# Kernel optimization log

Measured on AMD Instinct MI355X. Metric: run time of the kernel, lower is better.

Reference implementation:

```python
import jax, jax.numpy as jnp
import numpy as np
from jax import lax

N_CLS = 3
ALPHA = 2
NMS = True


def _make_level(key, B, A, D, H, W, P, counts):
    k1, k2, k3, k4, k5 = jax.random.split(key, 5)
    C = N_CLS * A
    logit = jax.random.normal(k1, (B, C, D, H, W), dtype=jnp.float32)
    # valid positive coords use d,h,w >= 1 so padded writes to (0,0,0,0) never collide
    a = jax.random.randint(k2, (B, P), 0, A)
    d = jax.random.randint(k3, (B, P), 1, D)
    h = jax.random.randint(k4, (B, P), 1, H)
    w = jax.random.randint(k5, (B, P), 1, W)
    labels = jax.random.randint(jax.random.fold_in(key, 7), (B, P), 0, N_CLS)
    valid = jnp.arange(P)[None, :] < jnp.asarray(counts)[:, None]  # [B,P]
    coord = jnp.stack([a, d, h, w], axis=-1)
    coord = jnp.where(valid[..., None], coord, -1).astype(jnp.int32)
    # ground-truth prob map: -1 = negative, class id (float) at positive voxels
    prob_gt = -jnp.ones((B, A, D, H, W), dtype=jnp.float32)
    cs = jnp.where(valid[..., None], coord, 0)
    b_idx = jnp.arange(B)[:, None]
    vals = jnp.where(valid, labels.astype(jnp.float32), -1.0)
    prob_gt = prob_gt.at[b_idx, cs[..., 0], cs[..., 1], cs[..., 2], cs[..., 3]].set(vals)
    return logit, prob_gt, coord


def setup_inputs() -> dict:
    key = jax.random.key(0)
    kA, kB = jax.random.split(key)
    logit0, prob_gt0, coord0 = _make_level(kA, 4, 3, 64, 64, 64, 128, [128, 64, 32, 0])
    logit1, prob_gt1, coord1 = _make_level(kB, 4, 3, 32, 32, 32, 128, [64, 16, 8, 128])
    weight_cls = jnp.array([1.0, 1.5, 2.0], dtype=jnp.float32)
    return {
        "logit0": logit0, "logit1": logit1,
        "prob_gt0": prob_gt0, "prob_gt1": prob_gt1,
        "coord0": coord0, "coord1": coord1,
        "weight_cls": weight_cls,
    }


def _level_loss(logit, prob_gt, coord_gt, weight_cls):
    B, C, D, H, W = logit.shape
    A = C // N_CLS
    logit = logit.reshape(B, N_CLS, A, D, H, W)
    logp = jax.nn.log_softmax(logit, axis=1)
    nll = -logp                      # [B,N_cls,A,D,H,W]
    prob = jnp.exp(logp)
    nll_neg = nll[:, 0]              # [B,A,D,H,W]
    prob_neg = prob[:, 0]
    negmask = (prob_gt == -1).astype(logit.dtype)
    if NMS:
        mp = lax.reduce_window(nll_neg, -jnp.inf, lax.max,
                               (1, 1, 3, 3, 3), (1, 1, 1, 1, 1),
                               [(0, 0), (0, 0), (1, 1), (1, 1), (1, 1)])
        negmask = negmask * lax.stop_gradient((mp == nll_neg).astype(logit.dtype))
    w_neg = (1.0 - lax.stop_gradient(prob_neg)) ** ALPHA * negmask
    loss_neg = jnp.sum(nll_neg * w_neg)
    count_neg = jnp.sum(w_neg)
    # positives: ragged coord gather, masked instead of per-sample python loop
    valid = coord_gt[:, :, 0] > -1                       # [B,P]
    c = jnp.where(valid[..., None], coord_gt, 0)         # safe coords
    a, d, h, w = c[..., 0], c[..., 1], c[..., 2], c[..., 3]
    b_idx = jnp.arange(B)[:, None]
    cls = prob_gt[b_idx, a, d, h, w].astype(jnp.int32)   # class id at positives
    cls = jnp.where(valid, cls, 0)
    p_t = prob[b_idx, cls, a, d, h, w]
    nll_t = nll[b_idx, cls, a, d, h, w]
    w_pos = ((1.0 - lax.stop_gradient(p_t)) ** ALPHA
             * weight_cls[cls] * valid.astype(logit.dtype))
    loss_pos = jnp.sum(nll_t * w_pos)
    count_pos = jnp.sum(w_pos)
    return loss_pos, loss_neg, count_pos, count_neg


def reference(logit0, logit1, prob_gt0, prob_gt1, coord0, coord1, weight_cls):
    lp0, ln0, cp0, cn0 = _level_loss(logit0, prob_gt0, coord0, weight_cls)
    lp1, ln1, cp1, cn1 = _level_loss(logit1, prob_gt1, coord1, weight_cls)
    return jnp.stack([lp0 + lp1, ln0 + ln1, cp0 + cp1, cn0 + cn1])
```

## Files before the change

### kernel.cpp

```cpp
#include <hip/hip_runtime.h>
#include <math.h>

#define NEG_INF (-INFINITY)

__device__ __forceinline__ float nll3(float l0, float l1, float l2) {
    float m = fmaxf(l0, fmaxf(l1, l2));
    float e0 = __expf(l0 - m);
    float e1 = __expf(l1 - m);
    float e2 = __expf(l2 - m);
    return __logf(e0 + e1 + e2) - (l0 - m);
}

template<int WL, int NR, int TD, int D, int H, int W>
__device__ void neg_strip(int uid, int lane,
                          const float* __restrict__ logit,
                          const float* __restrict__ pg,
                          float2* __restrict__ slot) {
    constexpr int NI = NR + 2;
    constexpr int HG = H / NR;
    constexpr int DT = D / TD;
    const int w = lane & (WL - 1);

    int t = uid;
    const int hg = t % HG; t /= HG;
    const int dt = t % DT; t /= DT;
    const int ba = t;
    const int a = ba % 3, b = ba / 3;
    const int h0 = hg * NR, d0 = dt * TD;

    const long S = (long)D * H * W;
    const float* lb  = logit + ((long)b * 9 + a) * S;
    const long  cs   = 3 * S;
    const float* pgb = pg + (long)ba * S;

    bool hv[NI]; int hoff[NI];
#pragma unroll
    for (int j = 0; j < NI; ++j) {
        int hh = h0 - 1 + j;
        hv[j] = (hh >= 0) && (hh < H);
        hoff[j] = hh * W + w;
    }

    float cur[NI][3] = {}, nxt[NI][3] = {};
    float vm0[NR], vm1[NR], c1r[NR], pgc[NR] = {}, pgn[NR] = {};
#pragma unroll
    for (int r = 0; r < NR; ++r) { vm0[r] = NEG_INF; vm1[r] = NEG_INF; c1r[r] = 0.f; }

    bool dv_cur = (d0 - 1 >= 0);
    if (dv_cur) {
        const float* p0 = lb + (long)(d0 - 1) * (H * W);
#pragma unroll
        for (int j = 0; j < NI; ++j) if (hv[j]) {
            const float* p = p0 + hoff[j];
            cur[j][0] = p[0]; cur[j][1] = p[cs]; cur[j][2] = p[2 * cs];
        }
    }

    float loss = 0.f, cnt = 0.f;

#pragma unroll
    for (int s = 0; s <= TD + 1; ++s) {
        const int d = d0 - 1 + s;
        const int dn = d + 1;
        const bool dv_nxt = (dn < D);
        if (s <= TD) {
            if (dv_nxt) {
                const float* p0 = lb + (long)dn * (H * W);
#pragma unroll
                for (int j = 0; j < NI; ++j) if (hv[j]) {
                    const float* p = p0 + hoff[j];
                    nxt[j][0] = p[0]; nxt[j][1] = p[cs]; nxt[j][2] = p[2 * cs];
                }
            }
            if (s >= 1) {
                const float* pp = pgb + (long)d * (H * W);
#pragma unroll
                for (int r = 0; r < NR; ++r)
                    pgn[r] = pp[(h0 + r) * W + w];
            }
        }

        float nv[NI], rm[NI];
#pragma unroll
        for (int j = 0; j < NI; ++j)
            nv[j] = (dv_cur && hv[j]) ? nll3(cur[j][0], cur[j][1], cur[j][2])
                                      : NEG_INF;
#pragma unroll
        for (int j = 0; j < NI; ++j) {
            float lf = __shfl(nv[j], lane - 1);
            float rt = __shfl(nv[j], lane + 1);
            lf = (w == 0)      ? NEG_INF : lf;
            rt = (w == WL - 1) ? NEG_INF : rt;
            rm[j] = fmaxf(nv[j], fmaxf(lf, rt));
        }
#pragma unroll
        for (int r = 0; r < NR; ++r) {
            float hw2 = fmaxf(rm[r], fmaxf(rm[r + 1], rm[r + 2]));
            float cc  = nv[r + 1];
            if (s >= 2 && pgc[r] == -1.0f) {
                float mp = fmaxf(vm0[r], fmaxf(vm1[r], hw2));
                if (mp == c1r[r]) {
                    float pn = __expf(-c1r[r]);
                    float wn = (1.f - pn) * (1.f - pn);
                    loss += c1r[r] * wn;
                    cnt  += wn;
                }
            }
            vm0[r] = vm1[r]; vm1[r] = hw2; c1r[r] = cc;
        }
#pragma unroll
        for (int r = 0; r < NR; ++r) pgc[r] = pgn[r];
        dv_cur = dv_nxt;
#pragma unroll
        for (int j = 0; j < NI; ++j) {
            cur[j][0] = nxt[j][0]; cur[j][1] = nxt[j][1]; cur[j][2] = nxt[j][2];
        }
    }

#pragma unroll
    for (int off = WL / 2; off > 0; off >>= 1) {
        loss += __shfl_down(loss, off, WL);
        cnt  += __shfl_down(cnt, off, WL);
    }
    if (w == 0) slot[uid] = make_float2(loss, cnt);
}

__device__ void pos_wave8(int sub, int lane,
                          const float* __restrict__ logit,
                          const float* __restrict__ prob_gt,
                          const int* __restrict__ coord,
                          const float* __restrict__ wcls,
                          float2* __restrict__ slot,
                          int D, int H, int W) {
    const int A = 3, P = 128;
    const long S = (long)D * H * W;
    const int i = sub * 64 + lane;
    const int b = i / P;
    const int* c = coord + (long)i * 4;
    const int a = c[0];
    float loss = 0.f, cnt = 0.f;
    if (a > -1) {
        const int d = c[1], h = c[2], w = c[3];
        const long s = ((long)d * H + h) * W + w;
        const int cls = (int)prob_gt[((long)b * A + a) * S + s];
        const float* lp = logit + ((long)b * 3 * A + a) * S + s;
        float l0 = lp[0];
        float l1 = lp[(long)A * S];
        float l2 = lp[2L * A * S];
        float m = fmaxf(l0, fmaxf(l1, l2));
        float e0 = __expf(l0 - m);
        float e1 = __expf(l1 - m);
        float e2 = __expf(l2 - m);
        float lsum = __logf(e0 + e1 + e2);
        float lc = (cls == 0) ? l0 : ((cls == 1) ? l1 : l2);
        float lpc = (lc - m) - lsum;
        float pt = __expf(lpc);
        float wp = (1.f - pt) * (1.f - pt) * wcls[cls];
        loss = (-lpc) * wp;
        cnt = wp;
    }
#pragma unroll
    for (int off = 32; off > 0; off >>= 1) {
        loss += __shfl_down(loss, off);
        cnt  += __shfl_down(cnt, off);
    }
    if (lane == 0) *slot = make_float2(loss, cnt);
}

#define NU0 6144
#define NW0 6144
#define NU1 1536
#define NW1 768
#define NWP 16
#define NSLOT (NU0 + NU1 + NWP)
#define TOTAL_WAVES (NW0 + NW1 + NWP)

__global__ __launch_bounds__(256)
void mega_kernel(const float* __restrict__ logit0,
                 const float* __restrict__ logit1,
                 const float* __restrict__ pg0,
                 const float* __restrict__ pg1,
                 const int* __restrict__ coord0,
                 const int* __restrict__ coord1,
                 const float* __restrict__ wcls,
                 float2* __restrict__ ws) {
    const int gw = blockIdx.x * 4 + (threadIdx.x >> 6);
    const int lane = threadIdx.x & 63;
    float2* wsneg = ws;
    float2* wspos = ws + (NU0 + NU1);
    if (gw < NW0) {
        neg_strip<64, 2, 4, 64, 64, 64>(gw, lane, logit0, pg0, wsneg);
    } else if (gw < NW0 + NW1) {
        const int u = (gw - NW0) * 2 + (lane >> 5);
        neg_strip<32, 2, 4, 32, 32, 32>(u, lane, logit1, pg1, wsneg + NU0);
    } else if (gw < NW0 + NW1 + 8) {
        const int sub = gw - NW0 - NW1;
        pos_wave8(sub, lane, logit0, pg0, coord0, wcls, wspos + sub, 64, 64, 64);
    } else if (gw < NW0 + NW1 + 16) {
        const int sub = gw - NW0 - NW1 - 8;
        pos_wave8(sub, lane, logit1, pg1, coord1, wcls, wspos + 8 + sub, 32, 32, 32);
    }
}

__global__ __launch_bounds__(1024)
void final_reduce(const float2* __restrict__ ws, float* __restrict__ out) {
    const float2* wsneg = ws;
    const float2* wspos = ws + (NU0 + NU1);
    float ln = 0.f, cn = 0.f, lp = 0.f, cp = 0.f;
    for (int i = threadIdx.x; i < NU0 + NU1; i += 1024) {
        float2 v = wsneg[i]; ln += v.x; cn += v.y;
    }
    if (threadIdx.x < NWP) {
        float2 v = wspos[threadIdx.x]; lp = v.x; cp = v.y;
    }
#pragma unroll
    for (int off = 32; off > 0; off >>= 1) {
        ln += __shfl_down(ln, off); cn += __shfl_down(cn, off);
        lp += __shfl_down(lp, off); cp += __shfl_down(cp, off);
    }
    __shared__ float s[16][4];
    const int wv = threadIdx.x >> 6;
    if ((threadIdx.x & 63) == 0) {
        s[wv][0] = ln; s[wv][1] = cn; s[wv][2] = lp; s[wv][3] = cp;
    }
    __syncthreads();
    if (threadIdx.x == 0) {
        float a = 0.f, b = 0.f, c = 0.f, d = 0.f;
#pragma unroll
        for (int i = 0; i < 16; ++i) {
            a += s[i][0]; b += s[i][1]; c += s[i][2]; d += s[i][3];
        }
        out[0] = c;
        out[1] = a;
        out[2] = d;
        out[3] = b;
    }
}

extern "C" void kernel_launch(void* const* d_in, const int* in_sizes, int n_in,
                              void* d_out, int out_size, void* d_ws, size_t ws_size,
                              hipStream_t stream) {
    const float* logit0   = (const float*)d_in[0];
    const float* logit1   = (const float*)d_in[1];
    const float* prob_gt0 = (const float*)d_in[2];
    const float* prob_gt1 = (const float*)d_in[3];
    const int*   coord0   = (const int*)d_in[4];
    const int*   coord1   = (const int*)d_in[5];
    const float* wcls     = (const float*)d_in[6];
    float* out = (float*)d_out;
    float2* ws = (float2*)d_ws;

    mega_kernel<<<TOTAL_WAVES / 4, 256, 0, stream>>>(
        logit0, logit1, prob_gt0, prob_gt1, coord0, coord1, wcls, ws);
    final_reduce<<<1, 1024, 0, stream>>>(ws, out);
}
```

Before: 106.7 us.

## Vectorize negative NMS strips with float4 loads and cross-row shuffles

Each lane now handles four consecutive W positions via float4 loads, and the wave is split into groups that each own one H row. The 3x3 H-neighbourhood max is formed with lane shuffles across groups instead of each lane loading all NR+2 rows. Level 1 now uses NR=4 so a full 64-lane wave is used per unit. The aim is fewer load instructions and less redundant row loading. In exchange it adds more shuffles and leaves some lanes idle, since only NR of the NR+2 groups accumulate.

```diff
diff --git a/kernel.cpp b/kernel.cpp
--- a/kernel.cpp
+++ b/kernel.cpp
@@ -11,15 +11,18 @@
     return __logf(e0 + e1 + e2) - (l0 - m);
 }
 
-template<int WL, int NR, int TD, int D, int H, int W>
-__device__ void neg_strip(int uid, int lane,
-                          const float* __restrict__ logit,
-                          const float* __restrict__ pg,
-                          float2* __restrict__ slot) {
+template<int W, int NR, int TD, int D, int H>
+__device__ void neg_strip_v(int uid, int lane,
+                            const float* __restrict__ logit,
+                            const float* __restrict__ pg,
+                            float2* __restrict__ slot) {
+    constexpr int LR = W / 4;
+    constexpr int NG = 64 / LR;
     constexpr int NI = NR + 2;
     constexpr int HG = H / NR;
     constexpr int DT = D / TD;
-    const int w = lane & (WL - 1);
+    const int q = lane % LR;
+    const int g = lane / LR;
 
     int t = uid;
     const int hg = t % HG; t /= HG;
@@ -33,27 +36,25 @@
     const long  cs   = 3 * S;
     const float* pgb = pg + (long)ba * S;
 
-    bool hv[NI]; int hoff[NI];
-#pragma unroll
-    for (int j = 0; j < NI; ++j) {
-        int hh = h0 - 1 + j;
-        hv[j] = (hh >= 0) && (hh < H);
-        hoff[j] = hh * W + w;
-    }
-
-    float cur[NI][3] = {}, nxt[NI][3] = {};
-    float vm0[NR], vm1[NR], c1r[NR], pgc[NR] = {}, pgn[NR] = {};
-#pragma unroll
-    for (int r = 0; r < NR; ++r) { vm0[r] = NEG_INF; vm1[r] = NEG_INF; c1r[r] = 0.f; }
-
-    bool dv_cur = (d0 - 1 >= 0);
-    if (dv_cur) {
-        const float* p0 = lb + (long)(d0 - 1) * (H * W);
-#pragma unroll
-        for (int j = 0; j < NI; ++j) if (hv[j]) {
-            const float* p = p0 + hoff[j];
-            cur[j][0] = p[0]; cur[j][1] = p[cs]; cur[j][2] = p[2 * cs];
-        }
+    const int jrow = h0 - 1 + g;
+    const bool hv = (jrow >= 0) && (jrow < H) && (g < NI);
+    const int hcl = min(max(jrow, 0), H - 1);
+    const int rowoff = hcl * W + 4 * q;
+    const int prowoff = (h0 + min(g, NR - 1)) * W + 4 * q;
+
+    float4 c0, c1v, c2, n0, n1, n2, pgn;
+    bool dvc = (d0 - 1 >= 0);
+    {
+        const float* p = lb + (long)max(d0 - 1, 0) * (H * W) + rowoff;
+        c0  = *(const float4*)(p);
+        c1v = *(const float4*)(p + cs);
+        c2  = *(const float4*)(p + 2 * cs);
+    }
+
+    float vm0[4], vm1[4], cc1[4], pgc[4];
+#pragma unroll
+    for (int i = 0; i < 4; ++i) {
+        vm0[i] = NEG_INF; vm1[i] = NEG_INF; cc1[i] = 0.f; pgc[i] = 0.f;
     }
 
     float loss = 0.f, cnt = 0.f;
@@ -61,68 +62,68 @@
 #pragma unroll
     for (int s = 0; s <= TD + 1; ++s) {
         const int d = d0 - 1 + s;
-        const int dn = d + 1;
-        const bool dv_nxt = (dn < D);
+        const bool dvn = (s <= TD - 1) || (d + 1 < D);
         if (s <= TD) {
-            if (dv_nxt) {
-                const float* p0 = lb + (long)dn * (H * W);
-#pragma unroll
-                for (int j = 0; j < NI; ++j) if (hv[j]) {
-                    const float* p = p0 + hoff[j];
-                    nxt[j][0] = p[0]; nxt[j][1] = p[cs]; nxt[j][2] = p[2 * cs];
-                }
-            }
-            if (s >= 1) {
-                const float* pp = pgb + (long)d * (H * W);
-#pragma unroll
-                for (int r = 0; r < NR; ++r)
-                    pgn[r] = pp[(h0 + r) * W + w];
-            }
-        }
-
-        float nv[NI], rm[NI];
-#pragma unroll
-        for (int j = 0; j < NI; ++j)
-            nv[j] = (dv_cur && hv[j]) ? nll3(cur[j][0], cur[j][1], cur[j][2])
-                                      : NEG_INF;
-#pragma unroll
-        for (int j = 0; j < NI; ++j) {
-            float lf = __shfl(nv[j], lane - 1);
-            float rt = __shfl(nv[j], lane + 1);
-            lf = (w == 0)      ? NEG_INF : lf;
-            rt = (w == WL - 1) ? NEG_INF : rt;
-            rm[j] = fmaxf(nv[j], fmaxf(lf, rt));
-        }
-#pragma unroll
-        for (int r = 0; r < NR; ++r) {
-            float hw2 = fmaxf(rm[r], fmaxf(rm[r + 1], rm[r + 2]));
-            float cc  = nv[r + 1];
-            if (s >= 2 && pgc[r] == -1.0f) {
-                float mp = fmaxf(vm0[r], fmaxf(vm1[r], hw2));
-                if (mp == c1r[r]) {
-                    float pn = __expf(-c1r[r]);
+            const float* p = lb + (long)min(d + 1, D - 1) * (H * W) + rowoff;
+            n0 = *(const float4*)(p);
+            n1 = *(const float4*)(p + cs);
+            n2 = *(const float4*)(p + 2 * cs);
+            pgn = *(const float4*)(pgb + (long)min(max(d, 0), D - 1) * (H * W)
+                                   + prowoff);
+        }
+
+        float nvv[4];
+        {
+            const bool vv = dvc && hv;
+            nvv[0] = vv ? nll3(c0.x, c1v.x, c2.x) : NEG_INF;
+            nvv[1] = vv ? nll3(c0.y, c1v.y, c2.y) : NEG_INF;
+            nvv[2] = vv ? nll3(c0.z, c1v.z, c2.z) : NEG_INF;
+            nvv[3] = vv ? nll3(c0.w, c1v.w, c2.w) : NEG_INF;
+        }
+
+        float le = __shfl(nvv[3], lane - 1);
+        float re = __shfl(nvv[0], lane + 1);
+        le = (q == 0)      ? NEG_INF : le;
+        re = (q == LR - 1) ? NEG_INF : re;
+        float rm[4];
+        rm[0] = fmaxf(le,     fmaxf(nvv[0], nvv[1]));
+        rm[1] = fmaxf(nvv[0], fmaxf(nvv[1], nvv[2]));
+        rm[2] = fmaxf(nvv[1], fmaxf(nvv[2], nvv[3]));
+        rm[3] = fmaxf(nvv[2], fmaxf(nvv[3], re));
+
+        float rmA[4], rmB[4], ctr[4];
+#pragma unroll
+        for (int i = 0; i < 4; ++i) {
+            rmA[i] = __shfl(rm[i],  lane + LR);
+            rmB[i] = __shfl(rm[i],  lane + 2 * LR);
+            ctr[i] = __shfl(nvv[i], lane + LR);
+        }
+
+#pragma unroll
+        for (int i = 0; i < 4; ++i) {
+            float hw2 = fmaxf(rm[i], fmaxf(rmA[i], rmB[i]));
+            if (s >= 2 && g < NR && pgc[i] == -1.0f) {
+                float mp = fmaxf(vm0[i], fmaxf(vm1[i], hw2));
+                if (mp == cc1[i]) {
+                    float pn = __expf(-cc1[i]);
                     float wn = (1.f - pn) * (1.f - pn);
-                    loss += c1r[r] * wn;
+                    loss += cc1[i] * wn;
                     cnt  += wn;
                 }
             }
-            vm0[r] = vm1[r]; vm1[r] = hw2; c1r[r] = cc;
-        }
-#pragma unroll
-        for (int r = 0; r < NR; ++r) pgc[r] = pgn[r];
-        dv_cur = dv_nxt;
-#pragma unroll
-        for (int j = 0; j < NI; ++j) {
-            cur[j][0] = nxt[j][0]; cur[j][1] = nxt[j][1]; cur[j][2] = nxt[j][2];
-        }
-    }
-
-#pragma unroll
-    for (int off = WL / 2; off > 0; off >>= 1) {
-        loss += __shfl_down(loss, off, WL);
-        cnt  += __shfl_down(cnt, off, WL);
-    }
-    if (w == 0) slot[uid] = make_float2(loss, cnt);
+            vm0[i] = vm1[i]; vm1[i] = hw2; cc1[i] = ctr[i];
+        }
+        pgc[0] = pgn.x; pgc[1] = pgn.y; pgc[2] = pgn.z; pgc[3] = pgn.w;
+        dvc = dvn;
+        c0 = n0; c1v = n1; c2 = n2;
+    }
+
+#pragma unroll
+    for (int off = 32; off > 0; off >>= 1) {
+        loss += __shfl_down(loss, off);
+        cnt  += __shfl_down(cnt, off);
+    }
+    if (lane == 0) slot[uid] = make_float2(loss, cnt);
 }
 
 __device__ void pos_wave8(int sub, int lane,
@@ -167,12 +168,10 @@
     if (lane == 0) *slot = make_float2(loss, cnt);
 }
 
-#define NU0 6144
 #define NW0 6144
-#define NU1 1536
 #define NW1 768
 #define NWP 16
-#define NSLOT (NU0 + NU1 + NWP)
+#define NUNEG (NW0 + NW1)
 #define TOTAL_WAVES (NW0 + NW1 + NWP)
 
 __global__ __launch_bounds__(256)
@@ -187,12 +186,11 @@
     const int gw = blockIdx.x * 4 + (threadIdx.x >> 6);
     const int lane = threadIdx.x & 63;
     float2* wsneg = ws;
-    float2* wspos = ws + (NU0 + NU1);
+    float2* wspos = ws + NUNEG;
     if (gw < NW0) {
-        neg_strip<64, 2, 4, 64, 64, 64>(gw, lane, logit0, pg0, wsneg);
+        neg_strip_v<64, 2, 4, 64, 64>(gw, lane, logit0, pg0, wsneg);
     } else if (gw < NW0 + NW1) {
-        const int u = (gw - NW0) * 2 + (lane >> 5);
-        neg_strip<32, 2, 4, 32, 32, 32>(u, lane, logit1, pg1, wsneg + NU0);
+        neg_strip_v<32, 4, 4, 32, 32>(gw - NW0, lane, logit1, pg1, wsneg + NW0);
     } else if (gw < NW0 + NW1 + 8) {
         const int sub = gw - NW0 - NW1;
         pos_wave8(sub, lane, logit0, pg0, coord0, wcls, wspos + sub, 64, 64, 64);
@@ -205,9 +203,9 @@
 __global__ __launch_bounds__(1024)
 void final_reduce(const float2* __restrict__ ws, float* __restrict__ out) {
     const float2* wsneg = ws;
-    const float2* wspos = ws + (NU0 + NU1);
+    const float2* wspos = ws + NUNEG;
     float ln = 0.f, cn = 0.f, lp = 0.f, cp = 0.f;
-    for (int i = threadIdx.x; i < NU0 + NU1; i += 1024) {
+    for (int i = threadIdx.x; i < NUNEG; i += 1024) {
         float2 v = wsneg[i]; ln += v.x; cn += v.y;
     }
     if (threadIdx.x < NWP) {
```

New measurement: 106.6 us. Within noise of the previous version (-0.1%).
